# Performance work log

Hardware: AMD Instinct MI355X
Metric: run time of the kernel (lower is better)

## Reference

```python
import math
import jax, jax.numpy as jnp
import numpy as np

X_DIM = 512
Y_DIM = 512
DS = 4
WH, WW = Y_DIM // DS, X_DIM // DS
RADIUS = 6          # search_radius
PATCH = 21          # patch_size
SIGMA = 1.0         # preprocess_sigma
DELTA = 0.2
MASK_TH = 0.05
RAIN_TH = 0.1


def _blur(x, sigma=SIGMA):
    # replicate-pad + depthwise 2D gaussian conv (matches _gaussian_blur2d)
    r = max(1, int(math.ceil(3.0 * sigma)))
    c = jnp.arange(-r, r + 1, dtype=x.dtype)
    k1 = jnp.exp(-(c * c) / (2.0 * sigma * sigma))
    k1 = k1 / jnp.sum(k1)
    k2 = jnp.outer(k1, k1)
    C = x.shape[1]
    kern = jnp.broadcast_to(k2[None, None], (C, 1, 2 * r + 1, 2 * r + 1))
    xp = jnp.pad(x, ((0, 0), (0, 0), (r, r), (r, r)), mode='edge')
    return jax.lax.conv_general_dilated(xp, kern, (1, 1), 'VALID',
                                        dimension_numbers=('NCHW', 'OIHW', 'NCHW'),
                                        feature_group_count=C)


def _resize(x, oh, ow):
    # torch bilinear, align_corners=False, no antialias
    ih, iw = x.shape[-2], x.shape[-1]
    def coords(o, i):
        s = (jnp.arange(o, dtype=jnp.float32) + 0.5) * (i / o) - 0.5
        s = jnp.maximum(s, 0.0)
        i0 = jnp.minimum(jnp.floor(s).astype(jnp.int32), i - 1)
        i1 = jnp.minimum(i0 + 1, i - 1)
        return i0, i1, s - i0.astype(jnp.float32)
    y0, y1, wy = coords(oh, ih)
    x0, x1, wx = coords(ow, iw)
    r0 = x[..., y0, :]
    r1 = x[..., y1, :]
    v00 = r0[..., x0]; v01 = r0[..., x1]
    v10 = r1[..., x0]; v11 = r1[..., x1]
    wy = wy[:, None]; wx = wx[None, :]
    return v00 * (1 - wy) * (1 - wx) + v01 * (1 - wy) * wx + v10 * wy * (1 - wx) + v11 * wy * wx


def _avg_pool(x, k):
    # avg_pool2d, stride 1, padding k//2, count_include_pad=True
    p = k // 2
    nd = x.ndim
    win = (1,) * (nd - 2) + (k, k)
    pads = ((0, 0),) * (nd - 2) + ((p, p), (p, p))
    s = jax.lax.reduce_window(x, 0.0, jax.lax.add, win, (1,) * nd, pads)
    return s / float(k * k)


def _prepare(f):
    w = jnp.log1p(jnp.maximum(f, 0.0))
    w = _resize(w, WH, WW)
    return _blur(w)


def _grid_sample_border(field, grid):
    # bilinear grid_sample, padding_mode='border', align_corners=True
    B, C, H, W = field.shape
    ix = jnp.clip((grid[..., 0] + 1.0) * 0.5 * (W - 1), 0.0, W - 1)
    iy = jnp.clip((grid[..., 1] + 1.0) * 0.5 * (H - 1), 0.0, H - 1)
    x0 = jnp.floor(ix).astype(jnp.int32); y0 = jnp.floor(iy).astype(jnp.int32)
    x1 = jnp.minimum(x0 + 1, W - 1); y1 = jnp.minimum(y0 + 1, H - 1)
    wx = (ix - x0)[..., None]; wy = (iy - y0)[..., None]
    b = jnp.arange(B)[:, None, None]
    v00 = field[b, :, y0, x0]; v01 = field[b, :, y0, x1]
    v10 = field[b, :, y1, x0]; v11 = field[b, :, y1, x1]  # each [B,H,W,C]
    out = v00 * (1 - wy) * (1 - wx) + v01 * (1 - wy) * wx + v10 * wy * (1 - wx) + v11 * wy * wx
    return jnp.transpose(out, (0, 3, 1, 2))


def setup_inputs() -> dict:
    key = jax.random.key(0)
    k1, k2, k3 = jax.random.split(key, 3)
    pred = jax.random.normal(k1, (16, 1, 512, 512), dtype=jnp.float32)
    target = jax.random.uniform(k2, (16, 1, 512, 512), dtype=jnp.float32)
    ref = jax.random.uniform(k3, (16, 1, 512, 512), dtype=jnp.float32)
    return {"pred": pred, "target": target, "ref": ref}


def reference(pred, target, ref):
    prev_w = _prepare(ref)      # [B,1,WH,WW]
    curr_w = _prepare(target)
    rain = (_resize(target, WH, WW) >= RAIN_TH).astype(jnp.float32)
    n = 2 * RADIUS + 1
    offs = jnp.arange(-RADIUS, RADIUS + 1)
    dys = jnp.repeat(offs, n)   # dy outer loop
    dxs = jnp.tile(offs, n)     # dx inner loop
    rows = jnp.arange(WH); cols = jnp.arange(WW)

    def shift_cost(dy, dx):
        # replicate-border shift of curr_w by (dy,dx), then local SSD (21x21 avg)
        sh = curr_w[:, :, jnp.clip(rows + dy, 0, WH - 1), :]
        sh = sh[:, :, :, jnp.clip(cols + dx, 0, WW - 1)]
        return _avg_pool((prev_w - sh) ** 2, PATCH)

    costs = jax.vmap(shift_cost)(dys, dxs)        # [S,B,1,WH,WW]
    best = jnp.argmin(costs, axis=0)[:, 0]        # [B,WH,WW] (first-min, matches torch)
    fx = dxs.astype(jnp.float32)[best][:, None] * rain   # [B,1,WH,WW]
    fy = dys.astype(jnp.float32)[best][:, None] * rain
    fx = _blur(fx) * rain
    fy = _blur(fy) * rain
    fx = _resize(fx, Y_DIM, X_DIM) * (X_DIM / WW)
    fy = _resize(fy, Y_DIM, X_DIM) * (Y_DIM / WH)

    yy, xx = jnp.meshgrid(jnp.linspace(-1.0, 1.0, Y_DIM),
                          jnp.linspace(-1.0, 1.0, X_DIM), indexing='ij')
    gx = xx[None] - fx[:, 0] * (2.0 / (X_DIM - 1))
    gy = yy[None] - fy[:, 0] * (2.0 / (Y_DIM - 1))
    teacher = jnp.maximum(_grid_sample_border(ref, jnp.stack([gx, gy], axis=-1)), 0.0)

    d = pred - teacher
    ad = jnp.abs(d)
    loss = jnp.where(ad < DELTA, 0.5 * d * d, DELTA * (ad - 0.5 * DELTA))  # huber
    mask = ((teacher > MASK_TH) | (target > MASK_TH)).astype(loss.dtype)
    return jnp.mean(loss * mask)
```

## Files before the change

### kernel.cpp

```cpp
#include <hip/hip_runtime.h>
#include <math.h>

#define BATCH 16
#define HR 512
#define LR 128
#define N_LR (BATCH*LR*LR)
#define N_HR (BATCH*HR*HR)
#define NSH 13
#define NSHIFT 169
#define TH 8
#define NW 8

__device__ __forceinline__ int clampi(int v, int lo, int hi){ return v<lo?lo:(v>hi?hi:v); }

__device__ __forceinline__ float gk(int t){
  const float e1 = 0.60653065971263342f;
  const float e2 = 0.13533528323661270f;
  const float e3 = 0.011108996538242306f;
  const float norm = 1.0f/(1.0f + 2.0f*(e1+e2+e3));
  int a = t < 0 ? -t : t;
  float v = (a==0) ? 1.0f : (a==1 ? e1 : (a==2 ? e2 : e3));
  return v*norm;
}

__global__ void k_downsample(const float* __restrict__ ref, const float* __restrict__ tar,
                             float* __restrict__ wref, float* __restrict__ wtar,
                             float* __restrict__ rain){
  int i = blockIdx.x*blockDim.x + threadIdx.x;
  if (i >= N_LR) return;
  int x = i & (LR-1); int y = (i >> 7) & (LR-1); int b = i >> 14;
  int base = b*HR*HR + (4*y+1)*HR + 4*x;
  float4 r1 = *(const float4*)(ref + base);
  float4 r2 = *(const float4*)(ref + base + HR);
  float4 t1 = *(const float4*)(tar + base);
  float4 t2 = *(const float4*)(tar + base + HR);
  float r00=r1.y, r01=r1.z, r10=r2.y, r11=r2.z;
  float t00=t1.y, t01=t1.z, t10=t2.y, t11=t2.z;
  wref[i] = 0.25f*(log1pf(fmaxf(r00,0.f))+log1pf(fmaxf(r01,0.f))
                 +log1pf(fmaxf(r10,0.f))+log1pf(fmaxf(r11,0.f)));
  wtar[i] = 0.25f*(log1pf(fmaxf(t00,0.f))+log1pf(fmaxf(t01,0.f))
                 +log1pf(fmaxf(t10,0.f))+log1pf(fmaxf(t11,0.f)));
  rain[i] = (0.25f*(t00+t01+t10+t11) >= 0.1f) ? 1.0f : 0.0f;
}

__global__ void k_blur2(const float* __restrict__ in0, const float* __restrict__ in1,
                        float* __restrict__ out0, float* __restrict__ out1,
                        const float* __restrict__ m0, const float* __restrict__ m1){
  const int z = blockIdx.z;
  const float* in  = z ? in1 : in0;
  float* out       = z ? out1 : out0;
  const float* msk = z ? m1 : m0;
  const int r0 = blockIdx.x * 16;
  const int bb = blockIdx.y;
  const int tid = threadIdx.x;
  const float* I = in + (bb<<14);
  __shared__ float raw[22][LR];
  __shared__ float hb[22][LR];
  for (int idx = tid; idx < 22*LR; idx += 256){
    int lr = idx >> 7, c = idx & (LR-1);
    int gr = clampi(r0 - 3 + lr, 0, LR-1);
    raw[lr][c] = I[(gr<<7) + c];
  }
  __syncthreads();
  for (int idx = tid; idx < 22*LR; idx += 256){
    int lr = idx >> 7, c = idx & (LR-1);
    float s = 0.f;
    #pragma unroll
    for (int t=-3;t<=3;++t) s += gk(t)*raw[lr][clampi(c+t,0,LR-1)];
    hb[lr][c] = s;
  }
  __syncthreads();
  for (int idx = tid; idx < 16*LR; idx += 256){
    int lr = idx >> 7, c = idx & (LR-1);
    int i = r0 + lr;
    float s = 0.f;
    #pragma unroll
    for (int t=-3;t<=3;++t) s += gk(t)*hb[clampi(i+t,0,LR-1) - (r0-3)][c];
    int gi = (bb<<14) + (i<<7) + c;
    if (msk) s *= msk[gi];
    out[gi] = s;
  }
}

template<int CTRL, int RM>
__device__ __forceinline__ float dpp_mov0(float x){
  return __int_as_float(__builtin_amdgcn_update_dpp(0, __float_as_int(x), CTRL, RM, 0xF, true));
}
__device__ __forceinline__ float prefix64(float x){
  x += dpp_mov0<0x111,0xF>(x);
  x += dpp_mov0<0x112,0xF>(x);
  x += dpp_mov0<0x114,0xF>(x);
  x += dpp_mov0<0x118,0xF>(x);
  x += dpp_mov0<0x142,0xA>(x);
  x += dpp_mov0<0x143,0xC>(x);
  return x;
}
__device__ __forceinline__ float bperm(int addr4, float v){
  return __int_as_float(__builtin_amdgcn_ds_bpermute(addr4, __float_as_int(v)));
}

struct TapCtx { int ia0, ib0, ia1, ib1; bool la0hi, lb0ok, lb1hi, selA, selB; };

__device__ __forceinline__ void horiz_update(const TapCtx& tc, float v0, float v1, int s,
                                             unsigned long long& k0ref, unsigned long long& k1ref){
  float pf0 = prefix64(v0);
  float pf1 = prefix64(v1);
  float T0 = __int_as_float(__builtin_amdgcn_readlane(__float_as_int(pf0), 63));
  float va = tc.selA ? pf0 : pf1;
  float vb = tc.selB ? pf0 : pf1;
  float a0 = bperm(tc.ia0, va) + (tc.la0hi ? T0 : 0.f);
  float b0 = tc.lb0ok ? bperm(tc.ib0, pf0) : 0.f;
  float a1 = bperm(tc.ia1, pf1) + T0;
  float b1 = bperm(tc.ib1, vb) + (tc.lb1hi ? T0 : 0.f);
  float c0 = fmaxf((a0 - b0) * (1.0f/441.0f), 0.f);
  float c1 = fmaxf((a1 - b1) * (1.0f/441.0f), 0.f);
  unsigned long long k0 = ((unsigned long long)__float_as_uint(c0) << 32) | (unsigned)s;
  unsigned long long k1 = ((unsigned long long)__float_as_uint(c1) << 32) | (unsigned)s;
  if (k0 < k0ref) k0ref = k0;
  if (k1 < k1ref) k1ref = k1;
}

__global__ void __launch_bounds__(512, 2)
k_cost_flow(const float* __restrict__ prev, const float* __restrict__ curr,
            const float* __restrict__ rain,
            float* __restrict__ fx, float* __restrict__ fy){
  const int r0 = blockIdx.x * TH;
  const int bb = blockIdx.y;
  const int tid = threadIdx.x;
  const int w = tid >> 6, lane = tid & 63;
  const float* P = prev + (bb<<14);
  const float* C = curr + (bb<<14);

  __shared__ float currT[40][LR];
  __shared__ unsigned long long mg[4][TH*LR];

  for (int idx = tid; idx < 40*LR; idx += 512){
    int lr = idx >> 7, c = idx & (LR-1);
    int gr = clampi(r0 - 16 + lr, 0, LR-1);
    currT[lr][c] = C[(gr<<7) + c];
  }

  float p0[28], p1[28];
  #pragma unroll
  for (int wr = 0; wr < 28; ++wr){
    int gr = r0 - 10 + wr;
    if (gr >= 0 && gr < LR){ p0[wr] = P[(gr<<7) + lane]; p1[wr] = P[(gr<<7) + lane + 64]; }
    else                   { p0[wr] = 0.f; p1[wr] = 0.f; }
  }
  __syncthreads();

  unsigned long long bk0[TH], bk1[TH];
  #pragma unroll
  for (int io = 0; io < TH; ++io){ bk0[io] = ~0ULL; bk1[io] = ~0ULL; }

  TapCtx tc;
  tc.ia0 = ((lane + 10) & 63) << 2;
  tc.ib0 = ((lane - 11) & 63) << 2;
  tc.ia1 = (min(lane + 10, 63)) << 2;
  tc.ib1 = ((lane + 53) & 63) << 2;
  tc.la0hi = (lane >= 54);
  tc.lb0ok = (lane >= 11);
  tc.lb1hi = (lane >= 11);
  tc.selA  = (lane >= 10);
  tc.selB  = (lane >= 53);

  const int t_lo = (NSHIFT * w) / NW;
  const int t_hi = (NSHIFT * (w+1)) / NW;

  int t = t_lo;
  while (t < t_hi){
    const int dxi  = t / NSH;
    const int dyi0 = t - dxi*NSH;
    const int ndy  = min(NSH - dyi0, t_hi - t);
    const int dx   = dxi - 6;
    const int c0   = clampi(lane + dx, 0, LR-1);
    const int c1   = clampi(lane + 64 + dx, 0, LR-1);
    float q0[28], q1[28];
    #pragma unroll
    for (int wr = 0; wr < 28; ++wr){
      q0[wr] = currT[wr + dyi0][c0];
      q1[wr] = currT[wr + dyi0][c1];
    }
    int s = dyi0*NSH + dxi;
    for (int rep = 0; rep < ndy; ++rep){
      float v0 = 0.f, v1 = 0.f;
      #pragma unroll
      for (int wr = 0; wr <= 20; ++wr){
        if (r0 - 10 + wr >= 0 && r0 - 10 + wr < LR){
          float d0 = p0[wr] - q0[wr];
          float d1 = p1[wr] - q1[wr];
          v0 = fmaf(d0, d0, v0);
          v1 = fmaf(d1, d1, v1);
        }
      }
      horiz_update(tc, v0, v1, s, bk0[0], bk1[0]);
      #pragma unroll
      for (int io = 1; io < TH; ++io){
        {
          const int wrA = io + 20;
          if (r0 - 10 + wrA < LR){
            float d0 = p0[wrA] - q0[wrA];
            float d1 = p1[wrA] - q1[wrA];
            v0 = fmaf(d0, d0, v0);
            v1 = fmaf(d1, d1, v1);
          }
          const int wrS = io - 1;
          if (r0 - 10 + wrS >= 0){
            float d0 = p0[wrS] - q0[wrS];
            float d1 = p1[wrS] - q1[wrS];
            v0 = fmaf(-d0, d0, v0);
            v1 = fmaf(-d1, d1, v1);
          }
        }
        horiz_update(tc, v0, v1, s, bk0[io], bk1[io]);
      }
      if (rep < ndy - 1){
        #pragma unroll
        for (int wr = 0; wr < 27; ++wr){ q0[wr] = q0[wr+1]; q1[wr] = q1[wr+1]; }
        q0[27] = currT[dyi0 + rep + 28][c0];
        q1[27] = currT[dyi0 + rep + 28][c1];
      }
      s += NSH;
    }
    t += ndy;
  }

  __syncthreads();
  const int g = w & 3;
  if (w < 4){
    #pragma unroll
    for (int io = 0; io < TH; ++io){
      mg[g][io*LR + lane]      = bk0[io];
      mg[g][io*LR + lane + 64] = bk1[io];
    }
  }
  __syncthreads();
  if (w >= 4){
    #pragma unroll
    for (int io = 0; io < TH; ++io){
      unsigned long long m0 = mg[g][io*LR + lane];
      unsigned long long m1 = mg[g][io*LR + lane + 64];
      mg[g][io*LR + lane]      = (bk0[io] < m0) ? bk0[io] : m0;
      mg[g][io*LR + lane + 64] = (bk1[io] < m1) ? bk1[io] : m1;
    }
  }
  __syncthreads();
  for (int p = tid; p < TH*LR; p += 512){
    unsigned long long k  = mg[0][p];
    unsigned long long k1 = mg[1][p]; if (k1 < k) k = k1;
    unsigned long long k2 = mg[2][p]; if (k2 < k) k = k2;
    unsigned long long k3 = mg[3][p]; if (k3 < k) k = k3;
    int s = (int)(k & 0xffffffffULL);
    int io = p >> 7, jj = p & (LR-1);
    int gi = (bb<<14) + ((r0+io)<<7) + jj;
    float r = rain[gi];
    fx[gi] = (float)(s % NSH - 6) * r;
    fy[gi] = (float)(s / NSH - 6) * r;
  }
}

__global__ void __launch_bounds__(256)
k_loss(const float* __restrict__ pred, const float* __restrict__ tar,
       const float* __restrict__ ref, const float* __restrict__ fxb,
       const float* __restrict__ fyb, float* __restrict__ out){
  const int t0 = blockIdx.x*256 + threadIdx.x;
  float acc = 0.f;
  #pragma unroll
  for (int it = 0; it < 2; ++it){
    const int gq  = t0 + it*524288;
    const int b   = gq >> 16;
    const int rem = gq & 65535;
    const int y   = rem >> 7;
    const int m   = rem & 127;
    const int n = y >> 2, ky = y & 3;
    int y0; float wy;
    if (ky < 2){ y0 = max(n-1, 0); wy = (n >= 1) ? (ky == 0 ? 0.625f : 0.875f) : 0.f; }
    else       { y0 = n;           wy = (ky == 2) ? 0.125f : 0.375f; }
    const int y1 = min(y0+1, LR-1);
    const int lb = b << 14;
    const float* FxR0 = fxb + lb + (y0<<7);
    const float* FxR1 = fxb + lb + (y1<<7);
    const float* FyR0 = fyb + lb + (y0<<7);
    const float* FyR1 = fyb + lb + (y1<<7);
    const int cA = max(m-1, 0), cB = m, cC = min(m+1, LR-1);
    float xA0 = FxR0[cA], xB0 = FxR0[cB], xC0 = FxR0[cC];
    float xA1 = FxR1[cA], xB1 = FxR1[cB], xC1 = FxR1[cC];
    float yA0 = FyR0[cA], yB0 = FyR0[cB], yC0 = FyR0[cC];
    float yA1 = FyR1[cA], yB1 = FyR1[cB], yC1 = FyR1[cC];
    const bool mh = (m >= 1);
    const int hb = (b<<18) + (y<<9) + (m<<2);
    float4 pd = *(const float4*)(pred + hb);
    float4 td = *(const float4*)(tar + hb);
    const float* R = ref + (b<<18);
    const float wy1 = 1.f - wy;
    #pragma unroll
    for (int k = 0; k < 4; ++k){
      float wx;
      float lo0, hi0, lo1, hi1, flo0, fhi0, flo1, fhi1;
      if (k < 2){
        wx = mh ? (k == 0 ? 0.625f : 0.875f) : 0.f;
        lo0 = mh ? xA0 : xB0;  hi0 = mh ? xB0 : xC0;
        lo1 = mh ? xA1 : xB1;  hi1 = mh ? xB1 : xC1;
        flo0 = mh ? yA0 : yB0; fhi0 = mh ? yB0 : yC0;
        flo1 = mh ? yA1 : yB1; fhi1 = mh ? yB1 : yC1;
      } else {
        wx = (k == 2) ? 0.125f : 0.375f;
        lo0 = xB0;  hi0 = xC0;  lo1 = xB1;  hi1 = xC1;
        flo0 = yB0; fhi0 = yC0; flo1 = yB1; fhi1 = yC1;
      }
      const float w00 = wy1*(1.f-wx), w01 = wy1*wx, w10 = wy*(1.f-wx), w11 = wy*wx;
      const float fxv = 4.f*(w00*lo0 + w01*hi0 + w10*lo1 + w11*hi1);
      const float fyv = 4.f*(w00*flo0 + w01*fhi0 + w10*flo1 + w11*fhi1);
      const int x = (m<<2) + k;
      float ix = fminf(fmaxf((float)x - fxv, 0.f), (float)(HR-1));
      float iy = fminf(fmaxf((float)y - fyv, 0.f), (float)(HR-1));
      int gx0 = (int)ix; int gx1 = min(gx0+1, HR-1); float gwx = ix - (float)gx0;
      int gy0 = (int)iy; int gy1 = min(gy0+1, HR-1); float gwy = iy - (float)gy0;
      float v00 = R[(gy0<<9)+gx0], v01 = R[(gy0<<9)+gx1];
      float v10 = R[(gy1<<9)+gx0], v11 = R[(gy1<<9)+gx1];
      float tt = v00*(1.f-gwy)*(1.f-gwx) + v01*(1.f-gwy)*gwx
               + v10*gwy*(1.f-gwx)       + v11*gwy*gwx;
      float teacher = fmaxf(tt, 0.f);
      float pk = ((const float*)&pd)[k];
      float tk = ((const float*)&td)[k];
      float d  = pk - teacher;
      float ad = fabsf(d);
      float l  = ad < 0.2f ? 0.5f*d*d : 0.2f*(ad - 0.1f);
      float mm = (teacher > 0.05f || tk > 0.05f) ? 1.f : 0.f;
      acc += l*mm;
    }
  }
  acc *= (1.0f/(float)N_HR);
  #pragma unroll
  for (int o = 32; o > 0; o >>= 1) acc += __shfl_down(acc, o, 64);
  __shared__ float wsum[4];
  int lane = threadIdx.x & 63, wv = threadIdx.x >> 6;
  if (lane == 0) wsum[wv] = acc;
  __syncthreads();
  if (threadIdx.x == 0) atomicAdd(out, wsum[0]+wsum[1]+wsum[2]+wsum[3]);
}

extern "C" void kernel_launch(void* const* d_in, const int* in_sizes, int n_in,
                              void* d_out, int out_size, void* d_ws, size_t ws_size,
                              hipStream_t stream){
  const float* pred = (const float*)d_in[0];
  const float* tar  = (const float*)d_in[1];
  const float* ref  = (const float*)d_in[2];
  float* out = (float*)d_out;
  float* w = (float*)d_ws;
  float* prevW = w + 0*N_LR;
  float* currW = w + 1*N_LR;
  float* rain  = w + 2*N_LR;
  float* fxb   = w + 3*N_LR;
  float* fyb   = w + 4*N_LR;
  float* dsA   = w + 5*N_LR;
  float* dsB   = w + 6*N_LR;

  hipMemsetAsync(d_out, 0, sizeof(float), stream);

  const int tb = 256, nb = (N_LR + tb - 1)/tb;
  k_downsample<<<nb, tb, 0, stream>>>(ref, tar, dsA, dsB, rain);
  k_blur2<<<dim3(8, BATCH, 2), tb, 0, stream>>>(dsA, dsB, prevW, currW, nullptr, nullptr);
  k_cost_flow<<<dim3(LR/TH, BATCH), 512, 0, stream>>>(prevW, currW, rain, dsA, dsB);
  k_blur2<<<dim3(8, BATCH, 2), tb, 0, stream>>>(dsA, dsB, fxb, fyb, rain, rain);
  k_loss<<<2048, tb, 0, stream>>>(pred, tar, ref, fxb, fyb, out);
}
```

Measured before the change: 191.2 us.

## Split shift search across two blocks, merge argmin keys in fused flow blur

The cost/flow kernel now splits the 169 shifts over two blocks per tile (grid z=2), and each block writes its packed (cost,shift) min keys to global memory. A new blur kernel merges the two key arrays, decodes the flow, applies the rain mask and blurs. Interior tiles also take a bounds-check-free specialisation of the inner loop, and launch bounds ask for 4 blocks per CU. The aim is more parallelism, since 256 blocks were too few for the GPU. The cost is redundant loading of the tile's current and previous windows in both blocks, extra 64-bit global traffic, and register pressure under the tighter launch bounds.

```diff
diff --git a/kernel.cpp b/kernel.cpp
--- a/kernel.cpp
+++ b/kernel.cpp
@@ -10,6 +10,9 @@
 #define NSHIFT 169
 #define TH 8
 #define NW 8
+#define NSLOT 16
+
+template<bool B> struct BoolC { static constexpr bool value = B; };
 
 __device__ __forceinline__ int clampi(int v, int lo, int hi){ return v<lo?lo:(v>hi?hi:v); }
 
@@ -44,12 +47,10 @@
 }
 
 __global__ void k_blur2(const float* __restrict__ in0, const float* __restrict__ in1,
-                        float* __restrict__ out0, float* __restrict__ out1,
-                        const float* __restrict__ m0, const float* __restrict__ m1){
+                        float* __restrict__ out0, float* __restrict__ out1){
   const int z = blockIdx.z;
   const float* in  = z ? in1 : in0;
   float* out       = z ? out1 : out0;
-  const float* msk = z ? m1 : m0;
   const int r0 = blockIdx.x * 16;
   const int bb = blockIdx.y;
   const int tid = threadIdx.x;
@@ -76,9 +77,48 @@
     float s = 0.f;
     #pragma unroll
     for (int t=-3;t<=3;++t) s += gk(t)*hb[clampi(i+t,0,LR-1) - (r0-3)][c];
+    out[(bb<<14) + (i<<7) + c] = s;
+  }
+}
+
+__global__ void k_blur2f(const unsigned long long* __restrict__ best0,
+                         const unsigned long long* __restrict__ best1,
+                         const float* __restrict__ rain,
+                         float* __restrict__ outx, float* __restrict__ outy){
+  const int z = blockIdx.z;
+  float* out = z ? outy : outx;
+  const int r0 = blockIdx.x * 16;
+  const int bb = blockIdx.y;
+  const int tid = threadIdx.x;
+  __shared__ float raw[22][LR];
+  __shared__ float hb[22][LR];
+  for (int idx = tid; idx < 22*LR; idx += 256){
+    int lr = idx >> 7, c = idx & (LR-1);
+    int gr = clampi(r0 - 3 + lr, 0, LR-1);
+    int gi = (bb<<14) + (gr<<7) + c;
+    unsigned long long k = best0[gi];
+    unsigned long long k1 = best1[gi]; if (k1 < k) k = k1;
+    int s = (int)(k & 0xffffffffULL);
+    int f = z ? (s / NSH - 6) : (s % NSH - 6);
+    raw[lr][c] = (float)f * rain[gi];
+  }
+  __syncthreads();
+  for (int idx = tid; idx < 22*LR; idx += 256){
+    int lr = idx >> 7, c = idx & (LR-1);
+    float s = 0.f;
+    #pragma unroll
+    for (int t=-3;t<=3;++t) s += gk(t)*raw[lr][clampi(c+t,0,LR-1)];
+    hb[lr][c] = s;
+  }
+  __syncthreads();
+  for (int idx = tid; idx < 16*LR; idx += 256){
+    int lr = idx >> 7, c = idx & (LR-1);
+    int i = r0 + lr;
+    float s = 0.f;
+    #pragma unroll
+    for (int t=-3;t<=3;++t) s += gk(t)*hb[clampi(i+t,0,LR-1) - (r0-3)][c];
     int gi = (bb<<14) + (i<<7) + c;
-    if (msk) s *= msk[gi];
-    out[gi] = s;
+    out[gi] = s * rain[gi];
   }
 }
 
@@ -120,12 +160,13 @@
   if (k1 < k1ref) k1ref = k1;
 }
 
-__global__ void __launch_bounds__(512, 2)
+__global__ void __launch_bounds__(512, 4)
 k_cost_flow(const float* __restrict__ prev, const float* __restrict__ curr,
-            const float* __restrict__ rain,
-            float* __restrict__ fx, float* __restrict__ fy){
+            unsigned long long* __restrict__ best0,
+            unsigned long long* __restrict__ best1){
   const int r0 = blockIdx.x * TH;
   const int bb = blockIdx.y;
+  const int z  = blockIdx.z;
   const int tid = threadIdx.x;
   const int w = tid >> 6, lane = tid & 63;
   const float* P = prev + (bb<<14);
@@ -164,66 +205,72 @@
   tc.selA  = (lane >= 10);
   tc.selB  = (lane >= 53);
 
-  const int t_lo = (NSHIFT * w) / NW;
-  const int t_hi = (NSHIFT * (w+1)) / NW;
-
-  int t = t_lo;
-  while (t < t_hi){
-    const int dxi  = t / NSH;
-    const int dyi0 = t - dxi*NSH;
-    const int ndy  = min(NSH - dyi0, t_hi - t);
-    const int dx   = dxi - 6;
-    const int c0   = clampi(lane + dx, 0, LR-1);
-    const int c1   = clampi(lane + 64 + dx, 0, LR-1);
-    float q0[28], q1[28];
-    #pragma unroll
-    for (int wr = 0; wr < 28; ++wr){
-      q0[wr] = currT[wr + dyi0][c0];
-      q1[wr] = currT[wr + dyi0][c1];
-    }
-    int s = dyi0*NSH + dxi;
-    for (int rep = 0; rep < ndy; ++rep){
-      float v0 = 0.f, v1 = 0.f;
+  const int slot = z*NW + w;
+  const int t_lo = (NSHIFT * slot) / NSLOT;
+  const int t_hi = (NSHIFT * (slot+1)) / NSLOT;
+
+  auto walk = [&](auto CHK){
+    constexpr bool chk = decltype(CHK)::value;
+    int t = t_lo;
+    while (t < t_hi){
+      const int dxi  = t / NSH;
+      const int dyi0 = t - dxi*NSH;
+      const int ndy  = min(NSH - dyi0, t_hi - t);
+      const int dx   = dxi - 6;
+      const int c0   = clampi(lane + dx, 0, LR-1);
+      const int c1   = clampi(lane + 64 + dx, 0, LR-1);
+      float q0[28], q1[28];
       #pragma unroll
-      for (int wr = 0; wr <= 20; ++wr){
-        if (r0 - 10 + wr >= 0 && r0 - 10 + wr < LR){
-          float d0 = p0[wr] - q0[wr];
-          float d1 = p1[wr] - q1[wr];
-          v0 = fmaf(d0, d0, v0);
-          v1 = fmaf(d1, d1, v1);
-        }
+      for (int wr = 0; wr < 28; ++wr){
+        q0[wr] = currT[wr + dyi0][c0];
+        q1[wr] = currT[wr + dyi0][c1];
       }
-      horiz_update(tc, v0, v1, s, bk0[0], bk1[0]);
-      #pragma unroll
-      for (int io = 1; io < TH; ++io){
-        {
-          const int wrA = io + 20;
-          if (r0 - 10 + wrA < LR){
-            float d0 = p0[wrA] - q0[wrA];
-            float d1 = p1[wrA] - q1[wrA];
+      int s = dyi0*NSH + dxi;
+      for (int rep = 0; rep < ndy; ++rep){
+        float v0 = 0.f, v1 = 0.f;
+        #pragma unroll
+        for (int wr = 0; wr <= 20; ++wr){
+          if (!chk || (r0 - 10 + wr >= 0 && r0 - 10 + wr < LR)){
+            float d0 = p0[wr] - q0[wr];
+            float d1 = p1[wr] - q1[wr];
             v0 = fmaf(d0, d0, v0);
             v1 = fmaf(d1, d1, v1);
           }
-          const int wrS = io - 1;
-          if (r0 - 10 + wrS >= 0){
-            float d0 = p0[wrS] - q0[wrS];
-            float d1 = p1[wrS] - q1[wrS];
-            v0 = fmaf(-d0, d0, v0);
-            v1 = fmaf(-d1, d1, v1);
+        }
+        horiz_update(tc, v0, v1, s, bk0[0], bk1[0]);
+        #pragma unroll
+        for (int io = 1; io < TH; ++io){
+          {
+            const int wrA = io + 20;
+            if (!chk || (r0 - 10 + wrA < LR)){
+              float d0 = p0[wrA] - q0[wrA];
+              float d1 = p1[wrA] - q1[wrA];
+              v0 = fmaf(d0, d0, v0);
+              v1 = fmaf(d1, d1, v1);
+            }
+            const int wrS = io - 1;
+            if (!chk || (r0 - 10 + wrS >= 0)){
+              float d0 = p0[wrS] - q0[wrS];
+              float d1 = p1[wrS] - q1[wrS];
+              v0 = fmaf(-d0, d0, v0);
+              v1 = fmaf(-d1, d1, v1);
+            }
           }
+          horiz_update(tc, v0, v1, s, bk0[io], bk1[io]);
         }
-        horiz_update(tc, v0, v1, s, bk0[io], bk1[io]);
+        if (rep < ndy - 1){
+          #pragma unroll
+          for (int wr = 0; wr < 27; ++wr){ q0[wr] = q0[wr+1]; q1[wr] = q1[wr+1]; }
+          q0[27] = currT[dyi0 + rep + 28][c0];
+          q1[27] = currT[dyi0 + rep + 28][c1];
+        }
+        s += NSH;
       }
-      if (rep < ndy - 1){
-        #pragma unroll
-        for (int wr = 0; wr < 27; ++wr){ q0[wr] = q0[wr+1]; q1[wr] = q1[wr+1]; }
-        q0[27] = currT[dyi0 + rep + 28][c0];
-        q1[27] = currT[dyi0 + rep + 28][c1];
-      }
-      s += NSH;
+      t += ndy;
     }
-    t += ndy;
-  }
+  };
+  if (r0 >= 16 && r0 <= 104) walk(BoolC<false>{});
+  else                       walk(BoolC<true>{});
 
   __syncthreads();
   const int g = w & 3;
@@ -245,17 +292,14 @@
     }
   }
   __syncthreads();
+  unsigned long long* best = z ? best1 : best0;
   for (int p = tid; p < TH*LR; p += 512){
     unsigned long long k  = mg[0][p];
     unsigned long long k1 = mg[1][p]; if (k1 < k) k = k1;
     unsigned long long k2 = mg[2][p]; if (k2 < k) k = k2;
     unsigned long long k3 = mg[3][p]; if (k3 < k) k = k3;
-    int s = (int)(k & 0xffffffffULL);
     int io = p >> 7, jj = p & (LR-1);
-    int gi = (bb<<14) + ((r0+io)<<7) + jj;
-    float r = rain[gi];
-    fx[gi] = (float)(s % NSH - 6) * r;
-    fy[gi] = (float)(s / NSH - 6) * r;
+    best[(bb<<14) + ((r0+io)<<7) + jj] = k;
   }
 }
 
@@ -355,13 +399,15 @@
   float* fyb   = w + 4*N_LR;
   float* dsA   = w + 5*N_LR;
   float* dsB   = w + 6*N_LR;
+  unsigned long long* best0 = (unsigned long long*)(w + 7*N_LR);
+  unsigned long long* best1 = best0 + N_LR;
 
   hipMemsetAsync(d_out, 0, sizeof(float), stream);
 
   const int tb = 256, nb = (N_LR + tb - 1)/tb;
   k_downsample<<<nb, tb, 0, stream>>>(ref, tar, dsA, dsB, rain);
-  k_blur2<<<dim3(8, BATCH, 2), tb, 0, stream>>>(dsA, dsB, prevW, currW, nullptr, nullptr);
-  k_cost_flow<<<dim3(LR/TH, BATCH), 512, 0, stream>>>(prevW, currW, rain, dsA, dsB);
-  k_blur2<<<dim3(8, BATCH, 2), tb, 0, stream>>>(dsA, dsB, fxb, fyb, rain, rain);
+  k_blur2<<<dim3(8, BATCH, 2), tb, 0, stream>>>(dsA, dsB, prevW, currW);
+  k_cost_flow<<<dim3(LR/TH, BATCH, 2), 512, 0, stream>>>(prevW, currW, best0, best1);
+  k_blur2f<<<dim3(8, BATCH, 2), tb, 0, stream>>>(best0, best1, rain, fxb, fyb);
   k_loss<<<2048, tb, 0, stream>>>(pred, tar, ref, fxb, fyb, out);
 }
```

Measured after the change: 494.1 us. 2.58x slower.

## Use 1024-thread cost blocks with register-lean sliding window and interior fast path

Applied to the files above, without the earlier changes.

Doubles the cost-flow block to 16 waves, so each wave handles fewer shifts. The per-thread prev and curr register windows shrink from 28 to 21 rows; the extra rows now come from a small shared prevL buffer and direct shared-memory curr reads. It also adds a template-specialised interior path that drops the boundary checks, replaces one bpermute index with an equivalent existing one, and reworks the final min-merge into four serialized rounds. The goal is lower register pressure and more in-flight waves, at the cost of more LDS traffic, extra barriers in the merge, and a launch-bounds change that may force register spilling.

```diff
diff --git a/kernel.cpp b/kernel.cpp
--- a/kernel.cpp
+++ b/kernel.cpp
@@ -9,7 +9,9 @@
 #define NSH 13
 #define NSHIFT 169
 #define TH 8
-#define NW 8
+#define NW 16
+
+template<bool B> struct BoolC { static constexpr bool value = B; };
 
 __device__ __forceinline__ int clampi(int v, int lo, int hi){ return v<lo?lo:(v>hi?hi:v); }
 
@@ -99,7 +101,7 @@
   return __int_as_float(__builtin_amdgcn_ds_bpermute(addr4, __float_as_int(v)));
 }
 
-struct TapCtx { int ia0, ib0, ia1, ib1; bool la0hi, lb0ok, lb1hi, selA, selB; };
+struct TapCtx { int ia0, ib0, ia1; bool la0hi, lb0ok, lb1hi, selA, selB; };
 
 __device__ __forceinline__ void horiz_update(const TapCtx& tc, float v0, float v1, int s,
                                              unsigned long long& k0ref, unsigned long long& k1ref){
@@ -111,7 +113,7 @@
   float a0 = bperm(tc.ia0, va) + (tc.la0hi ? T0 : 0.f);
   float b0 = tc.lb0ok ? bperm(tc.ib0, pf0) : 0.f;
   float a1 = bperm(tc.ia1, pf1) + T0;
-  float b1 = bperm(tc.ib1, vb) + (tc.lb1hi ? T0 : 0.f);
+  float b1 = bperm(tc.ib0, vb) + (tc.lb1hi ? T0 : 0.f);
   float c0 = fmaxf((a0 - b0) * (1.0f/441.0f), 0.f);
   float c1 = fmaxf((a1 - b1) * (1.0f/441.0f), 0.f);
   unsigned long long k0 = ((unsigned long long)__float_as_uint(c0) << 32) | (unsigned)s;
@@ -120,7 +122,7 @@
   if (k1 < k1ref) k1ref = k1;
 }
 
-__global__ void __launch_bounds__(512, 2)
+__global__ void __launch_bounds__(1024)
 k_cost_flow(const float* __restrict__ prev, const float* __restrict__ curr,
             const float* __restrict__ rain,
             float* __restrict__ fx, float* __restrict__ fy){
@@ -132,20 +134,26 @@
   const float* C = curr + (bb<<14);
 
   __shared__ float currT[40][LR];
+  __shared__ float prevL[7][LR];
   __shared__ unsigned long long mg[4][TH*LR];
 
-  for (int idx = tid; idx < 40*LR; idx += 512){
+  for (int idx = tid; idx < 40*LR; idx += 1024){
     int lr = idx >> 7, c = idx & (LR-1);
     int gr = clampi(r0 - 16 + lr, 0, LR-1);
     currT[lr][c] = C[(gr<<7) + c];
   }
-
-  float p0[28], p1[28];
-  #pragma unroll
-  for (int wr = 0; wr < 28; ++wr){
-    int gr = r0 - 10 + wr;
-    if (gr >= 0 && gr < LR){ p0[wr] = P[(gr<<7) + lane]; p1[wr] = P[(gr<<7) + lane + 64]; }
-    else                   { p0[wr] = 0.f; p1[wr] = 0.f; }
+  if (tid < 7*LR){
+    int j = tid >> 7, c = tid & (LR-1);
+    int gr = r0 + 11 + j;
+    prevL[j][c] = (gr < LR) ? P[(gr<<7) + c] : 0.f;
+  }
+
+  float p0[21], p1[21];
+  #pragma unroll
+  for (int k = 0; k < 21; ++k){
+    int gr = r0 - 10 + k;
+    if (gr >= 0 && gr < LR){ p0[k] = P[(gr<<7) + lane]; p1[k] = P[(gr<<7) + lane + 64]; }
+    else                   { p0[k] = 0.f; p1[k] = 0.f; }
   }
   __syncthreads();
 
@@ -157,7 +165,6 @@
   tc.ia0 = ((lane + 10) & 63) << 2;
   tc.ib0 = ((lane - 11) & 63) << 2;
   tc.ia1 = (min(lane + 10, 63)) << 2;
-  tc.ib1 = ((lane + 53) & 63) << 2;
   tc.la0hi = (lane >= 54);
   tc.lb0ok = (lane >= 11);
   tc.lb1hi = (lane >= 11);
@@ -167,85 +174,96 @@
   const int t_lo = (NSHIFT * w) / NW;
   const int t_hi = (NSHIFT * (w+1)) / NW;
 
-  int t = t_lo;
-  while (t < t_hi){
-    const int dxi  = t / NSH;
-    const int dyi0 = t - dxi*NSH;
-    const int ndy  = min(NSH - dyi0, t_hi - t);
-    const int dx   = dxi - 6;
-    const int c0   = clampi(lane + dx, 0, LR-1);
-    const int c1   = clampi(lane + 64 + dx, 0, LR-1);
-    float q0[28], q1[28];
-    #pragma unroll
-    for (int wr = 0; wr < 28; ++wr){
-      q0[wr] = currT[wr + dyi0][c0];
-      q1[wr] = currT[wr + dyi0][c1];
-    }
-    int s = dyi0*NSH + dxi;
-    for (int rep = 0; rep < ndy; ++rep){
-      float v0 = 0.f, v1 = 0.f;
+  auto walk = [&](auto CHK){
+    constexpr bool chk = decltype(CHK)::value;
+    int t = t_lo;
+    while (t < t_hi){
+      const int dxi  = t / NSH;
+      const int dyi0 = t - dxi*NSH;
+      const int ndy  = min(NSH - dyi0, t_hi - t);
+      const int dx   = dxi - 6;
+      const int c0   = clampi(lane + dx, 0, LR-1);
+      const int c1   = clampi(lane + 64 + dx, 0, LR-1);
+      float q0[21], q1[21];
       #pragma unroll
-      for (int wr = 0; wr <= 20; ++wr){
-        if (r0 - 10 + wr >= 0 && r0 - 10 + wr < LR){
-          float d0 = p0[wr] - q0[wr];
-          float d1 = p1[wr] - q1[wr];
-          v0 = fmaf(d0, d0, v0);
-          v1 = fmaf(d1, d1, v1);
-        }
+      for (int k = 0; k < 21; ++k){
+        q0[k] = currT[k + dyi0][c0];
+        q1[k] = currT[k + dyi0][c1];
       }
-      horiz_update(tc, v0, v1, s, bk0[0], bk1[0]);
-      #pragma unroll
-      for (int io = 1; io < TH; ++io){
-        {
-          const int wrA = io + 20;
-          if (r0 - 10 + wrA < LR){
-            float d0 = p0[wrA] - q0[wrA];
-            float d1 = p1[wrA] - q1[wrA];
+      int s = dyi0*NSH + dxi;
+      for (int rep = 0; rep < ndy; ++rep){
+        const int dyi = dyi0 + rep;
+        float v0 = 0.f, v1 = 0.f;
+        #pragma unroll
+        for (int k = 0; k <= 20; ++k){
+          if (!chk || (r0 - 10 + k >= 0 && r0 - 10 + k < LR)){
+            float d0 = p0[k] - q0[k];
+            float d1 = p1[k] - q1[k];
             v0 = fmaf(d0, d0, v0);
             v1 = fmaf(d1, d1, v1);
           }
-          const int wrS = io - 1;
-          if (r0 - 10 + wrS >= 0){
-            float d0 = p0[wrS] - q0[wrS];
-            float d1 = p1[wrS] - q1[wrS];
+        }
+        horiz_update(tc, v0, v1, s, bk0[0], bk1[0]);
+        float sav0 = 0.f, sav1 = 0.f;
+        #pragma unroll
+        for (int io = 1; io < TH; ++io){
+          float qa0 = currT[dyi + io + 20][c0];
+          float qa1 = currT[dyi + io + 20][c1];
+          if (io == 1){ sav0 = qa0; sav1 = qa1; }
+          if (!chk || (r0 + io + 10 < LR)){
+            float pa0 = prevL[io-1][lane];
+            float pa1 = prevL[io-1][lane + 64];
+            float d0 = pa0 - qa0;
+            float d1 = pa1 - qa1;
+            v0 = fmaf(d0, d0, v0);
+            v1 = fmaf(d1, d1, v1);
+          }
+          if (!chk || (r0 + io - 11 >= 0)){
+            float d0 = p0[io-1] - q0[io-1];
+            float d1 = p1[io-1] - q1[io-1];
             v0 = fmaf(-d0, d0, v0);
             v1 = fmaf(-d1, d1, v1);
           }
-        }
-        horiz_update(tc, v0, v1, s, bk0[io], bk1[io]);
+          horiz_update(tc, v0, v1, s, bk0[io], bk1[io]);
+        }
+        if (rep < ndy - 1){
+          #pragma unroll
+          for (int k = 0; k < 20; ++k){ q0[k] = q0[k+1]; q1[k] = q1[k+1]; }
+          q0[20] = sav0; q1[20] = sav1;
+        }
+        s += NSH;
       }
-      if (rep < ndy - 1){
+      t += ndy;
+    }
+  };
+  if (r0 >= 16 && r0 <= 104) walk(BoolC<false>{});
+  else                       walk(BoolC<true>{});
+
+  __syncthreads();
+  const int g = w & 3;
+  #pragma unroll
+  for (int round = 0; round < 4; ++round){
+    if ((w >> 2) == round){
+      if (round == 0){
         #pragma unroll
-        for (int wr = 0; wr < 27; ++wr){ q0[wr] = q0[wr+1]; q1[wr] = q1[wr+1]; }
-        q0[27] = currT[dyi0 + rep + 28][c0];
-        q1[27] = currT[dyi0 + rep + 28][c1];
+        for (int io = 0; io < TH; ++io){
+          mg[g][io*LR + lane]      = bk0[io];
+          mg[g][io*LR + lane + 64] = bk1[io];
+        }
+      } else {
+        #pragma unroll
+        for (int io = 0; io < TH; ++io){
+          unsigned long long m0 = mg[g][io*LR + lane];
+          unsigned long long m1 = mg[g][io*LR + lane + 64];
+          mg[g][io*LR + lane]      = (bk0[io] < m0) ? bk0[io] : m0;
+          mg[g][io*LR + lane + 64] = (bk1[io] < m1) ? bk1[io] : m1;
+        }
       }
-      s += NSH;
     }
-    t += ndy;
-  }
-
-  __syncthreads();
-  const int g = w & 3;
-  if (w < 4){
-    #pragma unroll
-    for (int io = 0; io < TH; ++io){
-      mg[g][io*LR + lane]      = bk0[io];
-      mg[g][io*LR + lane + 64] = bk1[io];
-    }
-  }
-  __syncthreads();
-  if (w >= 4){
-    #pragma unroll
-    for (int io = 0; io < TH; ++io){
-      unsigned long long m0 = mg[g][io*LR + lane];
-      unsigned long long m1 = mg[g][io*LR + lane + 64];
-      mg[g][io*LR + lane]      = (bk0[io] < m0) ? bk0[io] : m0;
-      mg[g][io*LR + lane + 64] = (bk1[io] < m1) ? bk1[io] : m1;
-    }
-  }
-  __syncthreads();
-  for (int p = tid; p < TH*LR; p += 512){
+    __syncthreads();
+  }
+  {
+    int p = tid;
     unsigned long long k  = mg[0][p];
     unsigned long long k1 = mg[1][p]; if (k1 < k) k = k1;
     unsigned long long k2 = mg[2][p]; if (k2 < k) k = k2;
@@ -361,7 +379,7 @@
   const int tb = 256, nb = (N_LR + tb - 1)/tb;
   k_downsample<<<nb, tb, 0, stream>>>(ref, tar, dsA, dsB, rain);
   k_blur2<<<dim3(8, BATCH, 2), tb, 0, stream>>>(dsA, dsB, prevW, currW, nullptr, nullptr);
-  k_cost_flow<<<dim3(LR/TH, BATCH), 512, 0, stream>>>(prevW, currW, rain, dsA, dsB);
+  k_cost_flow<<<dim3(LR/TH, BATCH), 1024, 0, stream>>>(prevW, currW, rain, dsA, dsB);
   k_blur2<<<dim3(8, BATCH, 2), tb, 0, stream>>>(dsA, dsB, fxb, fyb, rain, rain);
   k_loss<<<2048, tb, 0, stream>>>(pred, tar, ref, fxb, fyb, out);
 }
```

Measured after the change: 365.9 us. 1.91x slower.
